# Kernel tuning notes

Measured on AMD Instinct MI355X. Metric: run time of the kernel, lower is better.

The kernel has to match this reference:

```python
import jax, jax.numpy as jnp
import numpy as np
from jax import lax

SR = 44100  # sample_rate from __init__ default


def _log_scale(v, mn, mx):
    # Faithful to AudioParameter.validate_and_scale with scale='log':
    # clamp, map log(v) to [0,1] over [log(mn), log(mx)], then rescale LINEARLY to [mn, mx].
    v = float(np.clip(float(v), mn, mx))
    log_min = np.log(max(mn, 1e-6))
    log_max = np.log(mx)
    normalized = (np.log(max(v, 1e-6)) - log_min) / (log_max - log_min)
    return normalized * (mx - mn) + mn


def _eq_coeffs(frequency, gain, q, sr=SR):
    # Parameter validation/scaling (frequency, q are 'log' scale; gain is linear clamp)
    f = _log_scale(frequency, 20.0, 20000.0)
    g = float(np.clip(float(gain), -30.0, 30.0))
    Q = _log_scale(q, 0.1, 30.0)
    # torchaudio.functional.equalizer_biquad ('bell' peaking EQ) coefficients
    w0 = 2.0 * np.pi * f / sr
    A = 10.0 ** (g / 40.0)
    alpha = np.sin(w0) / (2.0 * Q)
    b0 = 1.0 + alpha * A
    b1 = -2.0 * np.cos(w0)
    b2 = 1.0 - alpha * A
    a0 = 1.0 + alpha / A
    a1 = b1
    a2 = 1.0 - alpha / A
    return (b0 / a0, b1 / a0, b2 / a0, a1 / a0, a2 / a0)


def _biquad(x, coefs):
    # Direct-form-I second-order IIR along last axis, vectorized over all leading dims.
    b0, b1, b2, a1, a2 = [jnp.asarray(c, x.dtype) for c in coefs]
    shp = x.shape
    xf = x.reshape(-1, shp[-1])  # (N, T)
    z = jnp.zeros((xf.shape[0],), x.dtype)

    def step(carry, xn):
        x1, x2, y1, y2 = carry
        yn = b0 * xn + b1 * x1 + b2 * x2 - a1 * y1 - a2 * y2
        return (xn, x1, yn, y1), yn

    _, ys = lax.scan(step, (z, z, z, z), xf.T)  # ys: (T, N)
    return ys.T.reshape(shp)


def setup_inputs() -> dict:
    key = jax.random.key(0)
    audio = jax.random.normal(key, (32, 2, 441000), dtype=jnp.float32)  # 10s stereo, batch 32
    return {"audio": audio, "frequency": 2000, "gain": 6, "q": 1}


def reference(audio, frequency, gain, q):
    # filter_type='bell' (default) -> torchaudio equalizer_biquad path
    coefs = _eq_coeffs(frequency, gain, q)
    return _biquad(audio, coefs)
```

## Files before the change

### kernel.cpp

```cpp
#include <hip/hip_runtime.h>
#include <math.h>

#ifndef M_PI
#define M_PI 3.14159265358979323846
#endif

#define T_LEN  441000
#define L      32
#define WARM   8
#define SEG_W  ((64 - WARM) * L)
#define WPC    ((T_LEN + SEG_W - 1) / SEG_W)
#define BLOCK  256
#define BLK_X  ((WPC + 3) / 4)


__device__ __forceinline__ double log_scale(double v, double mn, double mx) {
    v = fmin(fmax(v, mn), mx);
    double lmin = log(fmax(mn, 1e-6));
    double lmax = log(mx);
    double nrm = (log(fmax(v, 1e-6)) - lmin) / (lmax - lmin);
    return nrm * (mx - mn) + mn;
}

__global__ void eq_setup_kernel(const int* __restrict__ f_in,
                                const int* __restrict__ g_in,
                                const int* __restrict__ q_in,
                                float* __restrict__ ws) {
    double f = log_scale((double)f_in[0], 20.0, 20000.0);
    double g = fmin(fmax((double)g_in[0], -30.0), 30.0);
    double Q = log_scale((double)q_in[0], 0.1, 30.0);
    double w0 = 2.0 * M_PI * f / 44100.0;
    double A  = pow(10.0, g / 40.0);
    double al = sin(w0) / (2.0 * Q);
    double ca = cos(w0);
    double b0 = 1.0 + al * A;
    double b1 = -2.0 * ca;
    double b2 = 1.0 - al * A;
    double a0 = 1.0 + al / A;
    double B0 = b0 / a0, B1 = b1 / a0, B2 = b2 / a0;
    double A1 = b1 / a0, A2 = (1.0 - al / A) / a0;
    ws[0] = (float)B0; ws[1] = (float)B1; ws[2] = (float)B2;
    ws[3] = (float)A1; ws[4] = (float)A2;

    double p11 = -A1, p12 = -A2, p21 = 1.0, p22 = 0.0;
    for (int i = 0; i < 5; ++i) {
        double s11 = p11 * p11 + p12 * p21;
        double s12 = p11 * p12 + p12 * p22;
        double s21 = p21 * p11 + p22 * p21;
        double s22 = p21 * p12 + p22 * p22;
        p11 = s11; p12 = s12; p21 = s21; p22 = s22;
    }
    for (int j = 0; j < 6; ++j) {
        ws[5 + 4 * j + 0] = (float)p11;
        ws[5 + 4 * j + 1] = (float)p12;
        ws[5 + 4 * j + 2] = (float)p21;
        ws[5 + 4 * j + 3] = (float)p22;
        double s11 = p11 * p11 + p12 * p21;
        double s12 = p11 * p12 + p12 * p22;
        double s21 = p21 * p11 + p22 * p21;
        double s22 = p21 * p12 + p22 * p22;
        p11 = s11; p12 = s12; p21 = s21; p22 = s22;
    }
}

__global__ __launch_bounds__(BLOCK, 8) void eq_main_kernel(
        const float* __restrict__ x,
        const float* __restrict__ ws,
        float* __restrict__ y) {
    const int tid  = threadIdx.x;
    const int lane = tid & 63;
    const int wv   = tid >> 6;
    const int wave = blockIdx.x * (BLOCK / 64) + wv;
    if (wave * SEG_W >= T_LEN) return;
    const int ch   = blockIdx.y;

    const float b0 = ws[0], b1 = ws[1], b2 = ws[2], a1 = ws[3], a2 = ws[4];

    const float* __restrict__ xc = x + (size_t)ch * T_LEN;
    float*       __restrict__ yc = y + (size_t)ch * T_LEN;

    const int base = wave * SEG_W - WARM * L + lane * L;

    float xv[L], xm1, xm2;
    if (base >= 4 && base + L <= T_LEN) {
        const float4 vm = *reinterpret_cast<const float4*>(xc + base - 4);
        xm2 = vm.z; xm1 = vm.w;
#pragma unroll
        for (int q = 0; q < L / 4; ++q) {
            const float4 v = *reinterpret_cast<const float4*>(xc + base + 4 * q);
            xv[4 * q + 0] = v.x; xv[4 * q + 1] = v.y;
            xv[4 * q + 2] = v.z; xv[4 * q + 3] = v.w;
        }
    } else {
#pragma unroll
        for (int k = 0; k < L; ++k) {
            const int idx = base + k;
            xv[k] = (idx >= 0 && idx < T_LEN) ? xc[idx] : 0.f;
        }
        xm1 = (base - 1 >= 0 && base - 1 < T_LEN) ? xc[base - 1] : 0.f;
        xm2 = (base - 2 >= 0 && base - 2 < T_LEN) ? xc[base - 2] : 0.f;
    }

    float c0 = 0.f, c1 = 0.f;
    {
        float xk1 = xm1, xk2 = xm2;
#pragma unroll
        for (int k = 0; k < L; ++k) {
            const float xk = xv[k];
            const float t  = fmaf(b0, xk, fmaf(b1, xk1, b2 * xk2));
            const float yn = fmaf(-a1, c0, fmaf(-a2, c1, t));
            c1 = c0; c0 = yn;
            xk2 = xk1; xk1 = xk;
        }
    }

#pragma unroll
    for (int j = 0; j < 6; ++j) {
        const float m11 = ws[5 + 4 * j + 0], m12 = ws[5 + 4 * j + 1];
        const float m21 = ws[5 + 4 * j + 2], m22 = ws[5 + 4 * j + 3];
        const float d0 = __shfl_up(c0, 1u << j);
        const float d1 = __shfl_up(c1, 1u << j);
        if (lane >= (1 << j)) {
            c0 = fmaf(m11, d0, fmaf(m12, d1, c0));
            c1 = fmaf(m21, d0, fmaf(m22, d1, c1));
        }
    }

    float s0 = __shfl_up(c0, 1);
    float s1 = __shfl_up(c1, 1);
    if (lane == 0) { s0 = 0.f; s1 = 0.f; }

    if (lane >= WARM && base < T_LEN) {
        float p0 = s0, p1 = s1;
        float xk1 = xm1, xk2 = xm2;
        if (base + L <= T_LEN) {
#pragma unroll
            for (int q = 0; q < L / 4; ++q) {
                float ov[4];
#pragma unroll
                for (int r = 0; r < 4; ++r) {
                    const float xk = xv[4 * q + r];
                    const float t  = fmaf(b0, xk, fmaf(b1, xk1, b2 * xk2));
                    const float yn = fmaf(-a1, p0, fmaf(-a2, p1, t));
                    p1 = p0; p0 = yn;
                    xk2 = xk1; xk1 = xk;
                    ov[r] = yn;
                }
                *reinterpret_cast<float4*>(yc + base + 4 * q) =
                    make_float4(ov[0], ov[1], ov[2], ov[3]);
            }
        } else {
#pragma unroll
            for (int k = 0; k < L; ++k) {
                const float xk = xv[k];
                const float t  = fmaf(b0, xk, fmaf(b1, xk1, b2 * xk2));
                const float yn = fmaf(-a1, p0, fmaf(-a2, p1, t));
                p1 = p0; p0 = yn;
                xk2 = xk1; xk1 = xk;
                if (base + k < T_LEN) yc[base + k] = yn;
            }
        }
    }
}

extern "C" void kernel_launch(void* const* d_in, const int* in_sizes, int n_in,
                              void* d_out, int out_size, void* d_ws, size_t ws_size,
                              hipStream_t stream) {
    const float* x = (const float*)d_in[0];
    const int*   f = (const int*)d_in[1];
    const int*   g = (const int*)d_in[2];
    const int*   q = (const int*)d_in[3];
    float*       y  = (float*)d_out;
    float*       ws = (float*)d_ws;

    eq_setup_kernel<<<1, 1, 0, stream>>>(f, g, q, ws);

    const int nch = in_sizes[0] / T_LEN;
    dim3 grid(BLK_X, nch);
    eq_main_kernel<<<grid, dim3(BLOCK), 0, stream>>>(x, ws, y);
}
```

Baseline: 229.7 us.

## Replace serial recompute pass with impulse-response correction and shorten per-lane chunks

The second sequential biquad pass over each lane's chunk is replaced by a closed-form correction: the zero-state outputs are kept in registers and the carried-in state is added through precomputed powers of the state matrix stored in the workspace. The chunk length drops from 32 to 16 samples and the number of warm-up lanes rises from 8 to 16, so each wave emits fewer outputs and the grid grows. This removes a serial dependency chain in exchange for more redundant warm-up reads, extra registers for the stored outputs, and a smaller occupancy hint in the launch bounds.

```diff
diff --git a/kernel.cpp b/kernel.cpp
--- a/kernel.cpp
+++ b/kernel.cpp
@@ -5,13 +5,13 @@
 #define M_PI 3.14159265358979323846
 #endif
 
-#define T_LEN  441000
-#define L      32
-#define WARM   8
-#define SEG_W  ((64 - WARM) * L)
-#define WPC    ((T_LEN + SEG_W - 1) / SEG_W)
-#define BLOCK  256
-#define BLK_X  ((WPC + 3) / 4)
+#define T_LEN      441000
+#define L          16
+#define WARM_LANES 16
+#define OUT_W      ((64 - WARM_LANES) * L)
+#define WPC        ((T_LEN + OUT_W - 1) / OUT_W)
+#define BLOCK      256
+#define BLK_X      ((WPC + 3) / 4)
 
 
 __device__ __forceinline__ double log_scale(double v, double mn, double mx) {
@@ -42,8 +42,10 @@
     ws[0] = (float)B0; ws[1] = (float)B1; ws[2] = (float)B2;
     ws[3] = (float)A1; ws[4] = (float)A2;
 
-    double p11 = -A1, p12 = -A2, p21 = 1.0, p22 = 0.0;
-    for (int i = 0; i < 5; ++i) {
+    const double m11 = -A1, m12 = -A2, m21 = 1.0, m22 = 0.0;
+
+    double p11 = m11, p12 = m12, p21 = m21, p22 = m22;
+    for (int i = 0; i < 4; ++i) {
         double s11 = p11 * p11 + p12 * p21;
         double s12 = p11 * p12 + p12 * p22;
         double s21 = p21 * p11 + p22 * p21;
@@ -61,9 +63,20 @@
         double s22 = p21 * p12 + p22 * p22;
         p11 = s11; p12 = s12; p21 = s21; p22 = s22;
     }
+
+    double q11 = m11, q12 = m12, q21 = m21, q22 = m22;
+    for (int k = 0; k < 16; ++k) {
+        ws[29 + 2 * k] = (float)q11;
+        ws[30 + 2 * k] = (float)q12;
+        const double n11 = m11 * q11 + m12 * q21;
+        const double n12 = m11 * q12 + m12 * q22;
+        const double n21 = q11;
+        const double n22 = q12;
+        q11 = n11; q12 = n12; q21 = n21; q22 = n22;
+    }
 }
 
-__global__ __launch_bounds__(BLOCK, 8) void eq_main_kernel(
+__global__ __launch_bounds__(BLOCK, 6) void eq_main_kernel(
         const float* __restrict__ x,
         const float* __restrict__ ws,
         float* __restrict__ y) {
@@ -71,26 +84,28 @@
     const int lane = tid & 63;
     const int wv   = tid >> 6;
     const int wave = blockIdx.x * (BLOCK / 64) + wv;
-    if (wave * SEG_W >= T_LEN) return;
-    const int ch   = blockIdx.y;
+    if (wave >= WPC) return;
+    const int ch = blockIdx.y;
 
     const float b0 = ws[0], b1 = ws[1], b2 = ws[2], a1 = ws[3], a2 = ws[4];
 
     const float* __restrict__ xc = x + (size_t)ch * T_LEN;
     float*       __restrict__ yc = y + (size_t)ch * T_LEN;
 
-    const int base = wave * SEG_W - WARM * L + lane * L;
+    const int base = wave * OUT_W - WARM_LANES * L + lane * L;
 
     float xv[L], xm1, xm2;
     if (base >= 4 && base + L <= T_LEN) {
         const float4 vm = *reinterpret_cast<const float4*>(xc + base - 4);
         xm2 = vm.z; xm1 = vm.w;
-#pragma unroll
-        for (int q = 0; q < L / 4; ++q) {
-            const float4 v = *reinterpret_cast<const float4*>(xc + base + 4 * q);
-            xv[4 * q + 0] = v.x; xv[4 * q + 1] = v.y;
-            xv[4 * q + 2] = v.z; xv[4 * q + 3] = v.w;
-        }
+        const float4 v0 = *reinterpret_cast<const float4*>(xc + base + 0);
+        const float4 v1 = *reinterpret_cast<const float4*>(xc + base + 4);
+        const float4 v2 = *reinterpret_cast<const float4*>(xc + base + 8);
+        const float4 v3 = *reinterpret_cast<const float4*>(xc + base + 12);
+        xv[0]=v0.x;  xv[1]=v0.y;  xv[2]=v0.z;  xv[3]=v0.w;
+        xv[4]=v1.x;  xv[5]=v1.y;  xv[6]=v1.z;  xv[7]=v1.w;
+        xv[8]=v2.x;  xv[9]=v2.y;  xv[10]=v2.z; xv[11]=v2.w;
+        xv[12]=v3.x; xv[13]=v3.y; xv[14]=v3.z; xv[15]=v3.w;
     } else {
 #pragma unroll
         for (int k = 0; k < L; ++k) {
@@ -101,6 +116,7 @@
         xm2 = (base - 2 >= 0 && base - 2 < T_LEN) ? xc[base - 2] : 0.f;
     }
 
+    float yl[L];
     float c0 = 0.f, c1 = 0.f;
     {
         float xk1 = xm1, xk2 = xm2;
@@ -111,6 +127,7 @@
             const float yn = fmaf(-a1, c0, fmaf(-a2, c1, t));
             c1 = c0; c0 = yn;
             xk2 = xk1; xk1 = xk;
+            yl[k] = yn;
         }
     }
 
@@ -130,35 +147,24 @@
     float s1 = __shfl_up(c1, 1);
     if (lane == 0) { s0 = 0.f; s1 = 0.f; }
 
-    if (lane >= WARM && base < T_LEN) {
-        float p0 = s0, p1 = s1;
-        float xk1 = xm1, xk2 = xm2;
+    if (lane >= WARM_LANES && base < T_LEN) {
         if (base + L <= T_LEN) {
 #pragma unroll
             for (int q = 0; q < L / 4; ++q) {
-                float ov[4];
+                float o[4];
 #pragma unroll
                 for (int r = 0; r < 4; ++r) {
-                    const float xk = xv[4 * q + r];
-                    const float t  = fmaf(b0, xk, fmaf(b1, xk1, b2 * xk2));
-                    const float yn = fmaf(-a1, p0, fmaf(-a2, p1, t));
-                    p1 = p0; p0 = yn;
-                    xk2 = xk1; xk1 = xk;
-                    ov[r] = yn;
+                    const int k = 4 * q + r;
+                    o[r] = fmaf(ws[29 + 2 * k], s0, fmaf(ws[30 + 2 * k], s1, yl[k]));
                 }
                 *reinterpret_cast<float4*>(yc + base + 4 * q) =
-                    make_float4(ov[0], ov[1], ov[2], ov[3]);
+                    make_float4(o[0], o[1], o[2], o[3]);
             }
         } else {
 #pragma unroll
-            for (int k = 0; k < L; ++k) {
-                const float xk = xv[k];
-                const float t  = fmaf(b0, xk, fmaf(b1, xk1, b2 * xk2));
-                const float yn = fmaf(-a1, p0, fmaf(-a2, p1, t));
-                p1 = p0; p0 = yn;
-                xk2 = xk1; xk1 = xk;
-                if (base + k < T_LEN) yc[base + k] = yn;
-            }
+            for (int k = 0; k < L; ++k)
+                if (base + k < T_LEN)
+                    yc[base + k] = fmaf(ws[29 + 2 * k], s0, fmaf(ws[30 + 2 * k], s1, yl[k]));
         }
     }
 }
```

After: 215.4 us. 6.2% less time.
